# Performance work log

Measured on AMD Instinct MI355X. Metric: run time of the kernel, lower is better.

The kernel has to match this reference:

```python
import jax, jax.numpy as jnp
import numpy as np
import math

D_MODEL = 1024
NUM_HEADS = 16
HEAD_DIM = D_MODEL // NUM_HEADS
THETA = 10000.0
B, S = 2, 2048


def apply_rope(x, pos, theta=THETA):
    # x: [..., S, D]; pos: [S] int. Rotates consecutive (even, odd) pairs.
    d = x.shape[-1]
    inv_freq = theta ** (-jnp.arange(0, d, 2, dtype=jnp.float32) / d)  # [d/2]
    ang = pos.astype(jnp.float32)[:, None] * inv_freq[None, :]          # [S, d/2]
    cos, sin = jnp.cos(ang), jnp.sin(ang)
    xe = x[..., 0::2]
    xo = x[..., 1::2]
    re = xe * cos - xo * sin
    ro = xe * sin + xo * cos
    return jnp.stack([re, ro], axis=-1).reshape(x.shape)


def setup_inputs() -> dict:
    key = jax.random.key(0)
    ks = jax.random.split(key, 5)
    scale = 1.0 / math.sqrt(D_MODEL)
    return {
        "in_features": jax.random.normal(ks[0], (B, S, D_MODEL), dtype=jnp.float32),
        "token_positions": jnp.arange(S, dtype=jnp.int32),
        "wq": jax.random.normal(ks[1], (D_MODEL, D_MODEL), dtype=jnp.float32) * scale,
        "wk": jax.random.normal(ks[2], (D_MODEL, D_MODEL), dtype=jnp.float32) * scale,
        "wv": jax.random.normal(ks[3], (D_MODEL, D_MODEL), dtype=jnp.float32) * scale,
        "wo": jax.random.normal(ks[4], (D_MODEL, D_MODEL), dtype=jnp.float32) * scale,
    }


def reference(in_features, token_positions, wq, wk, wv, wo):
    x = in_features
    b, s, d = x.shape
    # Linear: y = x @ W.T  (weight stored as [out, in])
    def split_heads(y):
        return y.reshape(b, s, NUM_HEADS, HEAD_DIM).transpose(0, 2, 1, 3)  # [B,H,S,Dh]
    Q = split_heads(x @ wq.T)
    K = split_heads(x @ wk.T)
    V = split_heads(x @ wv.T)
    Q = apply_rope(Q, token_positions)
    K = apply_rope(K, token_positions)
    scores = jnp.einsum('bhqd,bhkd->bhqk', Q, K) / math.sqrt(HEAD_DIM)
    causal = jnp.tril(jnp.ones((s, s), dtype=bool))
    scores = jnp.where(causal, scores, -jnp.inf)
    weights = jax.nn.softmax(scores, axis=-1)
    out = jnp.einsum('bhqk,bhkd->bhqd', weights, V)  # [B,H,S,Dh]
    out = out.transpose(0, 2, 1, 3).reshape(b, s, d)
    return out @ wo.T
```

## Files before the change

### kernel.cpp

```cpp
#include <hip/hip_runtime.h>
#include <hip/hip_bf16.h>

typedef __bf16 bf16_t;
typedef __bf16 bf16x8 __attribute__((ext_vector_type(8)));
typedef __bf16 bf16x4 __attribute__((ext_vector_type(4)));
typedef float  f32x4  __attribute__((ext_vector_type(4)));
typedef float  f32x16 __attribute__((ext_vector_type(16)));
typedef unsigned int u32;
typedef unsigned int u32x2v __attribute__((ext_vector_type(2)));
typedef unsigned int u32x4v __attribute__((ext_vector_type(4)));

#define D_MODEL   1024
#define NQKV      3072
#define NQK       2048
#define NUM_HEADS 16
#define HEAD_DIM  64
#define SEQ       2048
#define BATCH     2
#define NTOK      4096
#define SM_SCALE_LOG2E 0.18033688011112042f
#define LOG2_THETA 13.287712379549449f
#define NEG_BIG  (-3.0e38f)

__device__ __forceinline__ int swz128(int row, int bytecol) {
  return row*128 + ((((bytecol>>4) ^ (row&7))<<4) | (bytecol & 15));
}

__device__ __forceinline__ void gload16(const void* g, void* l) {
  __builtin_amdgcn_global_load_lds((const __attribute__((address_space(1))) u32*)g,
                                   (__attribute__((address_space(3))) u32*)l, 16, 0, 0);
}

__device__ __forceinline__ u32 cvtpk_bf16(float a, float b) {
  u32 r;
  asm("v_cvt_pk_bf16_f32 %0, %1, %2" : "=v"(r) : "v"(a), "v"(b));
  return r;
}

__device__ __forceinline__ void plswap(u32 &a, u32 &b) {
#if __has_builtin(__builtin_amdgcn_permlane32_swap)
  u32x2v r = __builtin_amdgcn_permlane32_swap(a, b, false, false);
  a = r[0]; b = r[1];
#else
  u32 xa = __shfl_xor((unsigned)a, 32, 64);
  u32 xb = __shfl_xor((unsigned)b, 32, 64);
  bool hi = (threadIdx.x & 32) != 0;
  a = hi ? xb : a;
  b = hi ? b : xa;
#endif
}

__device__ const unsigned char slot_order144[144] = {
  72,74,76,77,78,79,
  64,66,68,69,70,71,73,75,
  56,58,60,61,62,63,65,67,
  48,50,52,53,54,55,57,59,
  14,15,40,42,44,45,46,47,49,51,115,119,121,123,125,127,129,130,131,133,
  134,135,136,137,138,139,140,141,142,143,
  12,13,32,34,36,37,38,39,41,43,83,87,89,91,93,95,97,98,99,101,
  102,103,104,105,106,107,108,109,110,111,112,113,114,116,117,118,120,122,124,126,
  128,132,
  10,11,24,26,28,29,30,31,33,35,80,81,82,84,85,86,88,90,92,94,96,100,
  8,9,16,18,20,21,22,23,25,27,
  6,7,17,19,
  4,5, 2,3, 0,1
};

__global__ void cvt_all(const float* __restrict__ x,  const float* __restrict__ wq,
                        const float* __restrict__ wk, const float* __restrict__ wv,
                        const float* __restrict__ wo,
                        bf16_t* __restrict__ xb, bf16_t* __restrict__ wqkv,
                        bf16_t* __restrict__ wob) {
  const int NX = NTOK*D_MODEL;
  const int NW = D_MODEL*D_MODEL;
  int i = (blockIdx.x*256 + threadIdx.x)*4;
  float4 v; bf16_t* dst;
  if (i < NX) { v = *reinterpret_cast<const float4*>(x + i); dst = xb + i; }
  else {
    int k = i - NX;
    if      (k <   NW) { v = *reinterpret_cast<const float4*>(wq + k);        dst = wqkv + k; }
    else if (k < 2*NW) { v = *reinterpret_cast<const float4*>(wk + k -   NW); dst = wqkv + k; }
    else if (k < 3*NW) { v = *reinterpret_cast<const float4*>(wv + k - 2*NW); dst = wqkv + k; }
    else               { v = *reinterpret_cast<const float4*>(wo + k - 3*NW); dst = wob + k - 3*NW; }
  }
  bf16x4 o; o[0]=(bf16_t)v.x; o[1]=(bf16_t)v.y; o[2]=(bf16_t)v.z; o[3]=(bf16_t)v.w;
  *reinterpret_cast<bf16x4*>(dst) = o;
}

template<typename OutT, bool QKV>
__global__ __launch_bounds__(256, 1) void gemm8(const bf16_t* __restrict__ A,
                                                const bf16_t* __restrict__ B,
                                                OutT* __restrict__ C,
                                                bf16_t* __restrict__ Vt,
                                                const int* __restrict__ pos,
                                                int M, int N, int K) {
  __shared__ __align__(16) char lds[4][32768];
  int tid = threadIdx.x;
  int n0 = blockIdx.x*128, m0 = blockIdx.y*128;
  int wid = tid>>6, lane = tid&63;
  int wr = wid>>1, wc = wid&1;
  int lr = lane&15, lg = lane>>4;

  const int nT = K >> 6;
  const int CN = QKV ? NQK : N;

  int srow = tid >> 3;
  int sc8  = (tid & 7) ^ (srow & 7);
  const bf16_t* ga = A + (size_t)(m0 + srow)*K + sc8*8;
  const bf16_t* gb = B + (size_t)(n0 + srow)*K + sc8*8;

  f32x4 acc[4][4];
  #pragma unroll
  for (int a=0;a<4;a++)
    #pragma unroll
    for (int b=0;b<4;b++) acc[a][b] = (f32x4){0.f,0.f,0.f,0.f};

  auto stage = [&](int t) {
    char* s = lds[t&3];
    int k0 = t << 6;
    #pragma unroll
    for (int g=0; g<4; g++)
      gload16(ga + (size_t)(g*32)*K + k0, s + g*4096 + tid*16);
    #pragma unroll
    for (int g=0; g<4; g++)
      gload16(gb + (size_t)(g*32)*K + k0, s + 16384 + g*4096 + tid*16);
  };

  stage(0);
  if (nT > 1) stage(1);
  asm volatile("s_waitcnt vmcnt(8)" ::: "memory");
  __builtin_amdgcn_sched_barrier(0);
  __builtin_amdgcn_s_barrier();

  for (int t = 0; t < nT; ++t) {
    char* sA = lds[t&3];
    char* sB = sA + 16384;

    bf16x8 bq[4][2], aq[2][2];
    #pragma unroll
    for (int ni=0; ni<4; ni++)
      #pragma unroll
      for (int ks=0; ks<2; ks++)
        bq[ni][ks] = *reinterpret_cast<const bf16x8*>(sB + swz128(wc*64+ni*16+lr, ks*64+lg*16));
    #pragma unroll
    for (int mi=0; mi<2; mi++)
      #pragma unroll
      for (int ks=0; ks<2; ks++)
        aq[mi][ks] = *reinterpret_cast<const bf16x8*>(sA + swz128(wr*64+mi*16+lr, ks*64+lg*16));
    if (t + 2 < nT) stage(t + 2);
    asm volatile("s_waitcnt lgkmcnt(0)" ::: "memory");
    __builtin_amdgcn_sched_barrier(0);
    __builtin_amdgcn_s_setprio(1);
    #pragma unroll
    for (int mi=0; mi<2; mi++)
      #pragma unroll
      for (int ni=0; ni<4; ni++)
        #pragma unroll
        for (int ks=0; ks<2; ks++)
          acc[mi][ni] = __builtin_amdgcn_mfma_f32_16x16x32_bf16(aq[mi][ks], bq[ni][ks], acc[mi][ni], 0, 0, 0);
    __builtin_amdgcn_s_setprio(0);
    __builtin_amdgcn_s_barrier();

    bf16x8 aq2[2][2];
    #pragma unroll
    for (int mi=0; mi<2; mi++)
      #pragma unroll
      for (int ks=0; ks<2; ks++)
        aq2[mi][ks] = *reinterpret_cast<const bf16x8*>(sA + swz128(wr*64+(mi+2)*16+lr, ks*64+lg*16));
    asm volatile("s_waitcnt lgkmcnt(0)" ::: "memory");
    __builtin_amdgcn_sched_barrier(0);
    __builtin_amdgcn_s_setprio(1);
    #pragma unroll
    for (int mi=0; mi<2; mi++)
      #pragma unroll
      for (int ni=0; ni<4; ni++)
        #pragma unroll
        for (int ks=0; ks<2; ks++)
          acc[mi+2][ni] = __builtin_amdgcn_mfma_f32_16x16x32_bf16(aq2[mi][ks], bq[ni][ks], acc[mi+2][ni], 0, 0, 0);
    __builtin_amdgcn_s_setprio(0);
    if (t + 2 < nT)      { asm volatile("s_waitcnt vmcnt(8)" ::: "memory"); }
    else if (t + 1 < nT) { asm volatile("s_waitcnt vmcnt(0)" ::: "memory"); }
    __builtin_amdgcn_sched_barrier(0);
    __builtin_amdgcn_s_barrier();
  }

  if (QKV && n0 < 2*D_MODEL) {
    bool isQ = (n0 < D_MODEL);
    float fr[4];
    #pragma unroll
    for (int ni=0; ni<4; ni++) {
      int j = ((wc*64 + ni*16 + lr) & 63) >> 1;
      fr[ni] = exp2f(-(float)j * (LOG2_THETA/32.0f));
    }
    #pragma unroll
    for (int mi=0; mi<4; mi++)
      #pragma unroll
      for (int r=0; r<4; r++) {
        int m = m0 + wr*64 + mi*16 + lg*4 + r;
        float pt = (float)pos[m & (SEQ-1)];
        #pragma unroll
        for (int ni=0; ni<4; ni++) {
          int n = n0 + wc*64 + ni*16 + lr;
          float v = acc[mi][ni][r];
          float p = __shfl_xor(v, 1, 64);
          float sv, cv;
          __sincosf(pt * fr[ni], &sv, &cv);
          float o = (n & 1) ? (p*sv + v*cv) : (v*cv - p*sv);
          if (isQ) o *= SM_SCALE_LOG2E;
          C[(size_t)m*CN + n] = (OutT)o;
        }
      }
  } else if (!QKV) {
    #pragma unroll
    for (int mi=0;mi<4;mi++)
      #pragma unroll
      for (int ni=0;ni<4;ni++)
        #pragma unroll
        for (int r=0;r<4;r++) {
          int m = m0 + wr*64 + mi*16 + lg*4 + r;
          int n = n0 + wc*64 + ni*16 + lr;
          C[(size_t)m*CN + n] = (OutT)acc[mi][ni][r];
        }
  } else {
    #pragma unroll
    for (int mi=0;mi<4;mi++)
      #pragma unroll
      for (int ni=0;ni<4;ni++)
        #pragma unroll
        for (int r=0;r<4;r++) {
          int m = m0 + wr*64 + mi*16 + lg*4 + r;
          int nl = n0 + wc*64 + ni*16 + lr - 2*D_MODEL;
          int h = nl >> 6, d = nl & 63;
          int bb = m >> 11, s = m & (SEQ-1);
          Vt[(((size_t)(bb*16 + h)*64 + d) << 11) + s] = (bf16_t)acc[mi][ni][r];
        }
  }
}

__global__ __launch_bounds__(64, 2) void attn14(const bf16_t* __restrict__ QK,
                                                const bf16_t* __restrict__ Vt,
                                                bf16_t* __restrict__ pOA,
                                                bf16_t* __restrict__ pOB,
                                                float2* __restrict__ pML) {
  __shared__ __align__(16) char sK[64*128];
  __shared__ __align__(16) char sV[64*128];

  int bh = blockIdx.x;
  int b = bh >> 4, h = bh & 15;
  int lane = threadIdx.x & 63;
  int q32 = lane & 31, hi = lane >> 5;
  int rsub = lane >> 3, sg = (lane & 7) ^ rsub;

  int s = slot_order144[blockIdx.y];
  int qw, t0, t1;
  if (s < 16) { qw = s; t0 = 0; t1 = (s >> 1) + 1; }
  else if (s < 80) {
    int e = s - 16;
    qw = 16 + (e >> 1);
    int nt = (qw >> 1) + 1, h0 = (nt + 1) >> 1;
    t0 = (e & 1) ? h0 : 0;
    t1 = (e & 1) ? nt : h0;
  } else {
    int e = s - 80;
    qw = 48 + (e >> 2);
    int nt = (qw >> 1) + 1, qq = e & 3;
    t0 = (nt * qq) >> 2;
    t1 = (nt * (qq + 1)) >> 2;
  }
  int qt = qw >> 1;
  int qg = qw*32 + q32;

  bf16x8 qf[4];
  const bf16_t* qrow = QK + (size_t)(b*SEQ + qw*32 + q32)*NQK + h*64 + hi*8;
  #pragma unroll
  for (int d=0; d<4; d++) qf[d] = *reinterpret_cast<const bf16x8*>(qrow + d*16);

  const bf16_t* kgb = QK + D_MODEL + ((size_t)(b*SEQ) + rsub)*NQK + h*64 + sg*8;
  const bf16_t* vgb = Vt + (size_t)bh*64*SEQ + (size_t)rsub*SEQ + sg*8;

  auto stageK = [&](int t) {
    const bf16_t* src = kgb + (size_t)t*64*NQK;
    #pragma unroll
    for (int c=0;c<8;c++)
      gload16(src + (size_t)(8*c)*NQK, sK + c*1024 + lane*16);
  };
  auto stageV = [&](int t) {
    const bf16_t* src = vgb + t*64;
    #pragma unroll
    for (int c=0;c<8;c++)
      gload16(src + (size_t)(8*c)*SEQ, sV + c*1024 + lane*16);
  };

  f32x16 O0 = (f32x16)0.0f, O1 = (f32x16)0.0f;
  float mrun = NEG_BIG, lrun = 0.f;

  stageK(t0); stageV(t0);
  asm volatile("s_waitcnt vmcnt(0)" ::: "memory");
  __builtin_amdgcn_sched_barrier(0);

  for (int ti = t0; ti < t1; ++ti) {
    bf16x8 k0f[4], k1f[4], v0f[4], v1f[4];
    #pragma unroll
    for (int ds=0; ds<4; ds++) {
      k0f[ds] = *reinterpret_cast<const bf16x8*>(sK + swz128(q32,    ds*32 + hi*16));
      k1f[ds] = *reinterpret_cast<const bf16x8*>(sK + swz128(32+q32, ds*32 + hi*16));
      v0f[ds] = *reinterpret_cast<const bf16x8*>(sV + swz128(q32,    ds*32 + hi*16));
      v1f[ds] = *reinterpret_cast<const bf16x8*>(sV + swz128(32+q32, ds*32 + hi*16));
    }
    asm volatile("s_waitcnt lgkmcnt(0)" ::: "memory");
    __builtin_amdgcn_sched_barrier(0);
    if (ti + 1 < t1) { stageK(ti + 1); stageV(ti + 1); }

    f32x16 p0 = (f32x16)0.0f, p1 = (f32x16)0.0f;
    __builtin_amdgcn_s_setprio(1);
    #pragma unroll
    for (int ds=0; ds<4; ds++) {
      p0 = __builtin_amdgcn_mfma_f32_32x32x16_bf16(k0f[ds], qf[ds], p0, 0, 0, 0);
      p1 = __builtin_amdgcn_mfma_f32_32x32x16_bf16(k1f[ds], qf[ds], p1, 0, 0, 0);
    }
    __builtin_amdgcn_s_setprio(0);

    if (ti == qt) {
      #pragma unroll
      for (int r=0; r<16; r++) {
        int kg = ti*64 + (r&3) + 8*(r>>2) + 4*hi;
        if (kg      > qg) p0[r] = NEG_BIG;
        if (kg + 32 > qg) p1[r] = NEG_BIG;
      }
    }

    float mx[8];
    #pragma unroll
    for (int r=0;r<8;r++) mx[r] = fmaxf(fmaxf(p0[r],p0[r+8]), fmaxf(p1[r],p1[r+8]));
    #pragma unroll
    for (int st=4; st>0; st>>=1)
      #pragma unroll
      for (int r=0;r<st;r++) mx[r] = fmaxf(mx[r], mx[r+st]);
    float mt = fmaxf(mx[0], __shfl_xor(mx[0], 32, 64));

    if (!__all(mt <= mrun + 8.0f)) {
      float mnew  = fmaxf(mrun, mt);
      float alpha = exp2f(mrun - mnew);
      lrun *= alpha;
      O0 *= alpha; O1 *= alpha;
      mrun = mnew;
    }
    #pragma unroll
    for (int r=0; r<16; r++) {
      p0[r] = exp2f(p0[r] - mrun);
      p1[r] = exp2f(p1[r] - mrun);
    }
    float sx[8];
    #pragma unroll
    for (int r=0;r<8;r++) sx[r] = (p0[r]+p0[r+8]) + (p1[r]+p1[r+8]);
    #pragma unroll
    for (int st=4; st>0; st>>=1)
      #pragma unroll
      for (int r=0;r<st;r++) sx[r] += sx[r+st];
    lrun += sx[0] + __shfl_xor(sx[0], 32, 64);

    u32 pk0[8], pk1[8];
    #pragma unroll
    for (int i2=0; i2<8; i2++) {
      pk0[i2] = cvtpk_bf16(p0[2*i2], p0[2*i2+1]);
      pk1[i2] = cvtpk_bf16(p1[2*i2], p1[2*i2+1]);
    }
    plswap(pk0[0], pk0[2]); plswap(pk0[1], pk0[3]);
    plswap(pk0[4], pk0[6]); plswap(pk0[5], pk0[7]);
    plswap(pk1[0], pk1[2]); plswap(pk1[1], pk1[3]);
    plswap(pk1[4], pk1[6]); plswap(pk1[5], pk1[7]);

    bf16x8 pa[4];
    pa[0] = __builtin_bit_cast(bf16x8, (u32x4v){pk0[0],pk0[1],pk0[2],pk0[3]});
    pa[1] = __builtin_bit_cast(bf16x8, (u32x4v){pk0[4],pk0[5],pk0[6],pk0[7]});
    pa[2] = __builtin_bit_cast(bf16x8, (u32x4v){pk1[0],pk1[1],pk1[2],pk1[3]});
    pa[3] = __builtin_bit_cast(bf16x8, (u32x4v){pk1[4],pk1[5],pk1[6],pk1[7]});

    __builtin_amdgcn_s_setprio(1);
    #pragma unroll
    for (int ks=0; ks<4; ks++) {
      O0 = __builtin_amdgcn_mfma_f32_32x32x16_bf16(v0f[ks], pa[ks], O0, 0, 0, 0);
      O1 = __builtin_amdgcn_mfma_f32_32x32x16_bf16(v1f[ks], pa[ks], O1, 0, 0, 0);
    }
    __builtin_amdgcn_s_setprio(0);

    if (ti + 1 < t1) {
      asm volatile("s_waitcnt vmcnt(0)" ::: "memory");
      __builtin_amdgcn_sched_barrier(0);
    }
  }

  bf16_t* base = (s < 112) ? (pOA + (size_t)(s*32 + bh)*2048)
                           : (pOB + (size_t)((s-112)*32 + bh)*2048);
  bf16_t* prow = base + q32*64;
  #pragma unroll
  for (int rg=0; rg<4; rg++) {
    int d0 = 8*rg + 4*hi;
    u32 a0 = cvtpk_bf16(O0[4*rg],   O0[4*rg+1]);
    u32 a1 = cvtpk_bf16(O0[4*rg+2], O0[4*rg+3]);
    *reinterpret_cast<u32x2v*>(prow + d0) = (u32x2v){a0, a1};
    u32 b0 = cvtpk_bf16(O1[4*rg],   O1[4*rg+1]);
    u32 b1 = cvtpk_bf16(O1[4*rg+2], O1[4*rg+3]);
    *reinterpret_cast<u32x2v*>(prow + 32 + d0) = (u32x2v){b0, b1};
  }
  if (hi == 0)
    pML[(s*32 + bh)*32 + q32] = make_float2(mrun, lrun);
}

__global__ __launch_bounds__(128) void combine(const bf16_t* __restrict__ pOA,
                                               const bf16_t* __restrict__ pOB,
                                               const float2* __restrict__ pML,
                                               bf16_t* __restrict__ Of) {
  int qw = blockIdx.x, bh = blockIdx.y;
  int b = bh >> 4, h = bh & 15;
  int t = threadIdx.x;
  int q = t >> 2, d0 = (t & 3) * 16;

  auto slotp = [&](int s) -> const bf16x8* {
    const bf16_t* base = (s < 112) ? (pOA + (size_t)(s*32 + bh)*2048)
                                   : (pOB + (size_t)((s-112)*32 + bh)*2048);
    return reinterpret_cast<const bf16x8*>(base + q*64 + d0);
  };
  auto mlv = [&](int s) -> float2 { return pML[(s*32 + bh)*32 + q]; };

  float r0[8], r1[8];
  #pragma unroll
  for (int i=0;i<8;i++) { r0[i]=0.f; r1[i]=0.f; }

  int s0, np;
  if (qw < 16)      { s0 = qw;               np = 1; }
  else if (qw < 48) { s0 = 16 + (qw-16)*2;   np = 2; }
  else              { s0 = 80 + (qw-48)*4;   np = 4; }

  float m = NEG_BIG;
  float2 ml[4];
  for (int i=0;i<np;i++) { ml[i] = mlv(s0+i); m = fmaxf(m, ml[i].x); }
  float lsum = 0.f, w[4];
  for (int i=0;i<np;i++) { w[i] = exp2f(ml[i].x - m); lsum += w[i]*ml[i].y; }
  float inv = 1.0f / lsum;

  for (int i=0;i<np;i++) {
    const bf16x8* sp = slotp(s0+i);
    bf16x8 o0 = sp[0], o1 = sp[1];
    float wi = w[i]*inv;
    #pragma unroll
    for (int j=0;j<8;j++) {
      r0[j] += wi*(float)o0[j];
      r1[j] += wi*(float)o1[j];
    }
  }

  bf16x8 y0, y1;
  #pragma unroll
  for (int j=0;j<8;j++) { y0[j]=(bf16_t)r0[j]; y1[j]=(bf16_t)r1[j]; }
  bf16x8* dst = reinterpret_cast<bf16x8*>(Of + ((size_t)(b*SEQ) + qw*32 + q)*D_MODEL + h*64 + d0);
  dst[0] = y0; dst[1] = y1;
}

extern "C" void kernel_launch(void* const* d_in, const int* in_sizes, int n_in,
                              void* d_out, int out_size, void* d_ws, size_t ws_size,
                              hipStream_t stream) {
  const float* x   = (const float*)d_in[0];
  const int*   pos = (const int*)  d_in[1];
  const float* wq  = (const float*)d_in[2];
  const float* wk  = (const float*)d_in[3];
  const float* wv  = (const float*)d_in[4];
  const float* wo  = (const float*)d_in[5];
  float* out = (float*)d_out;

  char* ws = (char*)d_ws;
  bf16_t* xb   = (bf16_t*)(ws);
  bf16_t* wqkv = (bf16_t*)(ws + ( 8u<<20));
  bf16_t* wob  = (bf16_t*)(ws + (14u<<20));
  bf16_t* QK   = (bf16_t*)(ws + (16u<<20));
  bf16_t* Vtb  = (bf16_t*)(ws + (40u<<20));
  bf16_t* pOA  = (bf16_t*)(ws);
  bf16_t* pOB  = (bf16_t*)(ws + (32u<<20));
  float2* pML  = (float2*)(ws + (36u<<20));
  bf16_t* Of   = (bf16_t*)(ws + (16u<<20));

  cvt_all<<<8*D_MODEL*D_MODEL/1024, 256, 0, stream>>>(x, wq, wk, wv, wo, xb, wqkv, wob);

  dim3 gqkv(NQKV/128, NTOK/128);
  gemm8<bf16_t, true><<<gqkv, 256, 0, stream>>>(xb, wqkv, QK, Vtb, pos, NTOK, NQKV, D_MODEL);

  dim3 gattn(32, 144);
  attn14<<<gattn, 64, 0, stream>>>(QK, Vtb, pOA, pOB, pML);

  dim3 gcomb(64, 32);
  combine<<<gcomb, 128, 0, stream>>>(pOA, pOB, pML, Of);

  dim3 gout(D_MODEL/128, NTOK/128);
  gemm8<float, false><<<gout, 256, 0, stream>>>(Of, wob, out, nullptr, nullptr, NTOK, D_MODEL, D_MODEL);
}
```

Measured before the change: 135.0 us.

## Enlarge QKV GEMM tile to 256x128 with 512 threads and triple buffering

Splits the shared GEMM template into two kernels. The QKV projection now uses 256x128 block tiles with 8 waves and a 3-stage LDS ring, so each B tile is reused across more rows and fewer blocks are launched. The Q/K output keeps the full NQKV row stride, and the split-attention partial buffers move into the output allocation. In exchange, LDS use rises to about 147KB per block, only one block fits per CU, and the pipeline is one stage shallower.

```diff
diff --git a/kernel.cpp b/kernel.cpp
--- a/kernel.cpp
+++ b/kernel.cpp
@@ -12,7 +12,6 @@
 
 #define D_MODEL   1024
 #define NQKV      3072
-#define NQK       2048
 #define NUM_HEADS 16
 #define HEAD_DIM  64
 #define SEQ       2048
@@ -87,22 +86,20 @@
   *reinterpret_cast<bf16x4*>(dst) = o;
 }
 
-template<typename OutT, bool QKV>
-__global__ __launch_bounds__(256, 1) void gemm8(const bf16_t* __restrict__ A,
-                                                const bf16_t* __restrict__ B,
-                                                OutT* __restrict__ C,
-                                                bf16_t* __restrict__ Vt,
-                                                const int* __restrict__ pos,
-                                                int M, int N, int K) {
-  __shared__ __align__(16) char lds[4][32768];
+__global__ __launch_bounds__(512, 1) void gemm_qkv(const bf16_t* __restrict__ A,
+                                                   const bf16_t* __restrict__ B,
+                                                   bf16_t* __restrict__ C,
+                                                   bf16_t* __restrict__ Vt,
+                                                   const int* __restrict__ pos) {
+  const int K = D_MODEL, N = NQKV;
+  __shared__ __align__(16) char lds[3][49152];
   int tid = threadIdx.x;
-  int n0 = blockIdx.x*128, m0 = blockIdx.y*128;
+  int n0 = blockIdx.x*128, m0 = blockIdx.y*256;
   int wid = tid>>6, lane = tid&63;
   int wr = wid>>1, wc = wid&1;
   int lr = lane&15, lg = lane>>4;
 
   const int nT = K >> 6;
-  const int CN = QKV ? NQK : N;
 
   int srow = tid >> 3;
   int sc8  = (tid & 7) ^ (srow & 7);
@@ -116,25 +113,25 @@
     for (int b=0;b<4;b++) acc[a][b] = (f32x4){0.f,0.f,0.f,0.f};
 
   auto stage = [&](int t) {
-    char* s = lds[t&3];
+    char* s = lds[t % 3];
     int k0 = t << 6;
     #pragma unroll
     for (int g=0; g<4; g++)
-      gload16(ga + (size_t)(g*32)*K + k0, s + g*4096 + tid*16);
-    #pragma unroll
-    for (int g=0; g<4; g++)
-      gload16(gb + (size_t)(g*32)*K + k0, s + 16384 + g*4096 + tid*16);
+      gload16(ga + (size_t)(g*64)*K + k0, s + g*8192 + tid*16);
+    #pragma unroll
+    for (int g=0; g<2; g++)
+      gload16(gb + (size_t)(g*64)*K + k0, s + 32768 + g*8192 + tid*16);
   };
 
   stage(0);
-  if (nT > 1) stage(1);
-  asm volatile("s_waitcnt vmcnt(8)" ::: "memory");
+  stage(1);
+  asm volatile("s_waitcnt vmcnt(6)" ::: "memory");
   __builtin_amdgcn_sched_barrier(0);
   __builtin_amdgcn_s_barrier();
 
   for (int t = 0; t < nT; ++t) {
-    char* sA = lds[t&3];
-    char* sB = sA + 16384;
+    char* sA = lds[t % 3];
+    char* sB = sA + 32768;
 
     bf16x8 bq[4][2], aq[2][2];
     #pragma unroll
@@ -178,13 +175,13 @@
         for (int ks=0; ks<2; ks++)
           acc[mi+2][ni] = __builtin_amdgcn_mfma_f32_16x16x32_bf16(aq2[mi][ks], bq[ni][ks], acc[mi+2][ni], 0, 0, 0);
     __builtin_amdgcn_s_setprio(0);
-    if (t + 2 < nT)      { asm volatile("s_waitcnt vmcnt(8)" ::: "memory"); }
+    if (t + 2 < nT)      { asm volatile("s_waitcnt vmcnt(6)" ::: "memory"); }
     else if (t + 1 < nT) { asm volatile("s_waitcnt vmcnt(0)" ::: "memory"); }
     __builtin_amdgcn_sched_barrier(0);
     __builtin_amdgcn_s_barrier();
   }
 
-  if (QKV && n0 < 2*D_MODEL) {
+  if (n0 < 2*D_MODEL) {
     bool isQ = (n0 < D_MODEL);
     float fr[4];
     #pragma unroll
@@ -207,20 +204,9 @@
           __sincosf(pt * fr[ni], &sv, &cv);
           float o = (n & 1) ? (p*sv + v*cv) : (v*cv - p*sv);
           if (isQ) o *= SM_SCALE_LOG2E;
-          C[(size_t)m*CN + n] = (OutT)o;
+          C[(size_t)m*N + n] = (bf16_t)o;
         }
       }
-  } else if (!QKV) {
-    #pragma unroll
-    for (int mi=0;mi<4;mi++)
-      #pragma unroll
-      for (int ni=0;ni<4;ni++)
-        #pragma unroll
-        for (int r=0;r<4;r++) {
-          int m = m0 + wr*64 + mi*16 + lg*4 + r;
-          int n = n0 + wc*64 + ni*16 + lr;
-          C[(size_t)m*CN + n] = (OutT)acc[mi][ni][r];
-        }
   } else {
     #pragma unroll
     for (int mi=0;mi<4;mi++)
@@ -237,7 +223,112 @@
   }
 }
 
-__global__ __launch_bounds__(64, 2) void attn14(const bf16_t* __restrict__ QK,
+__global__ __launch_bounds__(256, 1) void gemm_out(const bf16_t* __restrict__ A,
+                                                   const bf16_t* __restrict__ B,
+                                                   float* __restrict__ C,
+                                                   int M, int N, int K) {
+  __shared__ __align__(16) char lds[4][32768];
+  int tid = threadIdx.x;
+  int n0 = blockIdx.x*128, m0 = blockIdx.y*128;
+  int wid = tid>>6, lane = tid&63;
+  int wr = wid>>1, wc = wid&1;
+  int lr = lane&15, lg = lane>>4;
+
+  const int nT = K >> 6;
+
+  int srow = tid >> 3;
+  int sc8  = (tid & 7) ^ (srow & 7);
+  const bf16_t* ga = A + (size_t)(m0 + srow)*K + sc8*8;
+  const bf16_t* gb = B + (size_t)(n0 + srow)*K + sc8*8;
+
+  f32x4 acc[4][4];
+  #pragma unroll
+  for (int a=0;a<4;a++)
+    #pragma unroll
+    for (int b=0;b<4;b++) acc[a][b] = (f32x4){0.f,0.f,0.f,0.f};
+
+  auto stage = [&](int t) {
+    char* s = lds[t&3];
+    int k0 = t << 6;
+    #pragma unroll
+    for (int g=0; g<4; g++)
+      gload16(ga + (size_t)(g*32)*K + k0, s + g*4096 + tid*16);
+    #pragma unroll
+    for (int g=0; g<4; g++)
+      gload16(gb + (size_t)(g*32)*K + k0, s + 16384 + g*4096 + tid*16);
+  };
+
+  stage(0);
+  if (nT > 1) stage(1);
+  asm volatile("s_waitcnt vmcnt(8)" ::: "memory");
+  __builtin_amdgcn_sched_barrier(0);
+  __builtin_amdgcn_s_barrier();
+
+  for (int t = 0; t < nT; ++t) {
+    char* sA = lds[t&3];
+    char* sB = sA + 16384;
+
+    bf16x8 bq[4][2], aq[2][2];
+    #pragma unroll
+    for (int ni=0; ni<4; ni++)
+      #pragma unroll
+      for (int ks=0; ks<2; ks++)
+        bq[ni][ks] = *reinterpret_cast<const bf16x8*>(sB + swz128(wc*64+ni*16+lr, ks*64+lg*16));
+    #pragma unroll
+    for (int mi=0; mi<2; mi++)
+      #pragma unroll
+      for (int ks=0; ks<2; ks++)
+        aq[mi][ks] = *reinterpret_cast<const bf16x8*>(sA + swz128(wr*64+mi*16+lr, ks*64+lg*16));
+    if (t + 2 < nT) stage(t + 2);
+    asm volatile("s_waitcnt lgkmcnt(0)" ::: "memory");
+    __builtin_amdgcn_sched_barrier(0);
+    __builtin_amdgcn_s_setprio(1);
+    #pragma unroll
+    for (int mi=0; mi<2; mi++)
+      #pragma unroll
+      for (int ni=0; ni<4; ni++)
+        #pragma unroll
+        for (int ks=0; ks<2; ks++)
+          acc[mi][ni] = __builtin_amdgcn_mfma_f32_16x16x32_bf16(aq[mi][ks], bq[ni][ks], acc[mi][ni], 0, 0, 0);
+    __builtin_amdgcn_s_setprio(0);
+    __builtin_amdgcn_s_barrier();
+
+    bf16x8 aq2[2][2];
+    #pragma unroll
+    for (int mi=0; mi<2; mi++)
+      #pragma unroll
+      for (int ks=0; ks<2; ks++)
+        aq2[mi][ks] = *reinterpret_cast<const bf16x8*>(sA + swz128(wr*64+(mi+2)*16+lr, ks*64+lg*16));
+    asm volatile("s_waitcnt lgkmcnt(0)" ::: "memory");
+    __builtin_amdgcn_sched_barrier(0);
+    __builtin_amdgcn_s_setprio(1);
+    #pragma unroll
+    for (int mi=0; mi<2; mi++)
+      #pragma unroll
+      for (int ni=0; ni<4; ni++)
+        #pragma unroll
+        for (int ks=0; ks<2; ks++)
+          acc[mi+2][ni] = __builtin_amdgcn_mfma_f32_16x16x32_bf16(aq2[mi][ks], bq[ni][ks], acc[mi+2][ni], 0, 0, 0);
+    __builtin_amdgcn_s_setprio(0);
+    if (t + 2 < nT)      { asm volatile("s_waitcnt vmcnt(8)" ::: "memory"); }
+    else if (t + 1 < nT) { asm volatile("s_waitcnt vmcnt(0)" ::: "memory"); }
+    __builtin_amdgcn_sched_barrier(0);
+    __builtin_amdgcn_s_barrier();
+  }
+
+  #pragma unroll
+  for (int mi=0;mi<4;mi++)
+    #pragma unroll
+    for (int ni=0;ni<4;ni++)
+      #pragma unroll
+      for (int r=0;r<4;r++) {
+        int m = m0 + wr*64 + mi*16 + lg*4 + r;
+        int n = n0 + wc*64 + ni*16 + lr;
+        C[(size_t)m*N + n] = acc[mi][ni][r];
+      }
+}
+
+__global__ __launch_bounds__(64, 2) void attn14(const bf16_t* __restrict__ QKV,
                                                 const bf16_t* __restrict__ Vt,
                                                 bf16_t* __restrict__ pOA,
                                                 bf16_t* __restrict__ pOB,
@@ -271,18 +362,18 @@
   int qg = qw*32 + q32;
 
   bf16x8 qf[4];
-  const bf16_t* qrow = QK + (size_t)(b*SEQ + qw*32 + q32)*NQK + h*64 + hi*8;
+  const bf16_t* qrow = QKV + (size_t)(b*SEQ + qw*32 + q32)*NQKV + h*64 + hi*8;
   #pragma unroll
   for (int d=0; d<4; d++) qf[d] = *reinterpret_cast<const bf16x8*>(qrow + d*16);
 
-  const bf16_t* kgb = QK + D_MODEL + ((size_t)(b*SEQ) + rsub)*NQK + h*64 + sg*8;
+  const bf16_t* kgb = QKV + D_MODEL + ((size_t)(b*SEQ) + rsub)*NQKV + h*64 + sg*8;
   const bf16_t* vgb = Vt + (size_t)bh*64*SEQ + (size_t)rsub*SEQ + sg*8;
 
   auto stageK = [&](int t) {
-    const bf16_t* src = kgb + (size_t)t*64*NQK;
+    const bf16_t* src = kgb + (size_t)t*64*NQKV;
     #pragma unroll
     for (int c=0;c<8;c++)
-      gload16(src + (size_t)(8*c)*NQK, sK + c*1024 + lane*16);
+      gload16(src + (size_t)(8*c)*NQKV, sK + c*1024 + lane*16);
   };
   auto stageV = [&](int t) {
     const bf16_t* src = vgb + t*64;
@@ -472,24 +563,24 @@
   bf16_t* xb   = (bf16_t*)(ws);
   bf16_t* wqkv = (bf16_t*)(ws + ( 8u<<20));
   bf16_t* wob  = (bf16_t*)(ws + (14u<<20));
-  bf16_t* QK   = (bf16_t*)(ws + (16u<<20));
+  bf16_t* QKV  = (bf16_t*)(ws + (16u<<20));
   bf16_t* Vtb  = (bf16_t*)(ws + (40u<<20));
   bf16_t* pOA  = (bf16_t*)(ws);
-  bf16_t* pOB  = (bf16_t*)(ws + (32u<<20));
-  float2* pML  = (float2*)(ws + (36u<<20));
+  bf16_t* pOB  = (bf16_t*)(d_out);
+  float2* pML  = (float2*)((char*)d_out + (4u<<20));
   bf16_t* Of   = (bf16_t*)(ws + (16u<<20));
 
   cvt_all<<<8*D_MODEL*D_MODEL/1024, 256, 0, stream>>>(x, wq, wk, wv, wo, xb, wqkv, wob);
 
-  dim3 gqkv(NQKV/128, NTOK/128);
-  gemm8<bf16_t, true><<<gqkv, 256, 0, stream>>>(xb, wqkv, QK, Vtb, pos, NTOK, NQKV, D_MODEL);
+  dim3 gqkv(NQKV/128, NTOK/256);
+  gemm_qkv<<<gqkv, 512, 0, stream>>>(xb, wqkv, QKV, Vtb, pos);
 
   dim3 gattn(32, 144);
-  attn14<<<gattn, 64, 0, stream>>>(QK, Vtb, pOA, pOB, pML);
+  attn14<<<gattn, 64, 0, stream>>>(QKV, Vtb, pOA, pOB, pML);
 
   dim3 gcomb(64, 32);
   combine<<<gcomb, 128, 0, stream>>>(pOA, pOB, pML, Of);
 
   dim3 gout(D_MODEL/128, NTOK/128);
-  gemm8<float, false><<<gout, 256, 0, stream>>>(Of, wob, out, nullptr, nullptr, NTOK, D_MODEL, D_MODEL);
-}
+  gemm_out<<<gout, 256, 0, stream>>>(Of, wob, out, NTOK, D_MODEL, D_MODEL);
+}
```

Measured after the change: 130.8 us. 3.2% less time.
